# Performance work log

Measured on AMD Instinct MI355X. Metric: run time of the kernel, lower is better.

## Reference

```python
import jax, jax.numpy as jnp
import numpy as np

N = 50000      # nodes
E = 800000     # edges (before self-loops)
IN = 256       # in_channels
HID = 16       # hidden_channels per head
HEADS = 8
OUT = 64       # out_channels (classes)
NEG_SLOPE = 0.2  # PyG GATConv leaky_relu slope


def setup_inputs() -> dict:
    key = jax.random.key(0)
    ks = jax.random.split(key, 10)
    x = jax.random.normal(ks[0], (N, IN), jnp.float32)
    edge_index = jax.random.randint(ks[1], (2, E), 0, N, dtype=jnp.int32)
    g = lambda k, shape: jax.random.normal(k, shape, jnp.float32) * (1.0 / np.sqrt(shape[0]))
    W1 = g(ks[2], (IN, HEADS * HID))
    a_src1 = jax.random.normal(ks[3], (HEADS, HID), jnp.float32) * 0.1
    a_dst1 = jax.random.normal(ks[4], (HEADS, HID), jnp.float32) * 0.1
    b1 = jnp.zeros((HEADS * HID,), jnp.float32)
    W2 = g(ks[5], (HEADS * HID, OUT))
    a_src2 = jax.random.normal(ks[6], (1, OUT), jnp.float32) * 0.1
    a_dst2 = jax.random.normal(ks[7], (1, OUT), jnp.float32) * 0.1
    b2 = jnp.zeros((OUT,), jnp.float32)
    return {"x": x, "edge_index": edge_index, "W1": W1, "a_src1": a_src1,
            "a_dst1": a_dst1, "b1": b1, "W2": W2, "a_src2": a_src2,
            "a_dst2": a_dst2, "b2": b2}


def gat_conv(x, src, dst, W, a_s, a_d, b, heads, concat):
    # x: [n, f]; edges src->dst; attention softmax over incoming edges of dst
    n = x.shape[0]
    h = (x @ W).reshape(n, heads, -1)                 # [n, H, d]
    al_s = jnp.einsum('nhd,hd->nh', h, a_s)           # [n, H]
    al_d = jnp.einsum('nhd,hd->nh', h, a_d)
    e = jax.nn.leaky_relu(al_s[src] + al_d[dst], negative_slope=NEG_SLOPE)  # [E, H]
    m = jax.ops.segment_max(e, dst, num_segments=n)   # stable scatter-softmax
    ex = jnp.exp(e - m[dst])
    den = jax.ops.segment_sum(ex, dst, num_segments=n)
    alpha = ex / (den[dst] + 1e-16)                   # [E, H]
    out = jax.ops.segment_sum(h[src] * alpha[:, :, None], dst, num_segments=n)  # [n, H, d]
    out = out.reshape(n, -1) if concat else out.mean(axis=1)
    return out + b


def reference(x, edge_index, W1, a_src1, a_dst1, b1, W2, a_src2, a_dst2, b2):
    # inference mode: dropout disabled. PyG GATConv adds self-loops by default.
    n = x.shape[0]
    loop = jnp.arange(n, dtype=edge_index.dtype)
    ei = jnp.concatenate([edge_index, jnp.stack([loop, loop])], axis=1)
    src, dst = ei[0], ei[1]
    h = gat_conv(x, src, dst, W1, a_src1, a_dst1, b1, HEADS, True)
    h = jax.nn.elu(h)
    h = gat_conv(h, src, dst, W2, a_src2, a_dst2, b2, 1, False)
    return jax.nn.log_softmax(h, axis=1)
```

## Files before the change

kernel.cpp:

```cpp
#include <hip/hip_runtime.h>
#include <hip/hip_bf16.h>


typedef __attribute__((ext_vector_type(8))) short short8;
typedef __attribute__((ext_vector_type(4))) float f4;
typedef __attribute__((ext_vector_type(2))) float float2v;

#define NCHUNK 64
#define NRANGE 4
#define RSIZE 16384
#define CONVB 80

#define A1PAD 72
#define B1PAD 264
#define G2PAD 136

__device__ __forceinline__ unsigned short f2bf(float f) {
  unsigned int u = __builtin_bit_cast(unsigned int, f);
  u += 0x7fffu + ((u >> 16) & 1u);
  return (unsigned short)(u >> 16);
}
__device__ __forceinline__ float bf2f(unsigned short h) {
  unsigned int u = ((unsigned int)h) << 16;
  return __builtin_bit_cast(float, u);
}

__device__ __forceinline__ unsigned char f2fp8(float f) {
  unsigned int u = __builtin_bit_cast(unsigned int, f);
  unsigned int s = (u >> 24) & 0x80u;
  float a = fabsf(f);
  a = fminf(a, 448.f);
  if (a < 0.015625f) {
    int m = (int)rintf(a * 512.f);
    return (unsigned char)(s | (unsigned)m);
  }
  unsigned int ub = __builtin_bit_cast(unsigned int, a);
  ub += 0xFFFFFu + ((ub >> 20) & 1u);
  unsigned int e = (ub >> 23) - 120u;
  unsigned int m = (ub >> 20) & 7u;
  if (e > 15u) { e = 15u; m = 6u; }
  return (unsigned char)(s | (e << 3) | m);
}

__global__ __launch_bounds__(512) void hist_kernel(const int* __restrict__ ei,
                                                   int* __restrict__ hist,
                                                   const float* __restrict__ W1,
                                                   const float* __restrict__ W2,
                                                   unsigned short* __restrict__ Wt1,
                                                   unsigned short* __restrict__ Wt2,
                                                   int E, int N, int ET, int CS) {
  if (blockIdx.x >= NCHUNK * NRANGE) {
    int i = (blockIdx.x - NCHUNK * NRANGE) * 512 + threadIdx.x;
    if (i < 128 * 256) {
      int n = i >> 8, k = i & 255;
      Wt1[i] = f2bf(W1[k * 128 + n]);
    } else {
      int j = i - 128 * 256;
      if (j < 64 * 128) {
        int n = j >> 7, k = j & 127;
        Wt2[j] = f2bf(W2[k * 64 + n]);
      }
    }
    return;
  }
  __shared__ int lh[RSIZE];
  const int c = blockIdx.x & (NCHUNK - 1);
  const int r = blockIdx.x >> 6;
  const int base = r * RSIZE;
  for (int i = threadIdx.x; i < RSIZE; i += 512) lh[i] = 0;
  __syncthreads();
  const int e0 = c * CS, e1 = min(e0 + CS, ET);
  for (int e = e0 + threadIdx.x; e < e1; e += 512) {
    int d = (e < E) ? ei[E + e] : (e - E);
    unsigned dl = (unsigned)(d - base);
    if (dl < RSIZE) atomicAdd(&lh[dl], 1);
  }
  __syncthreads();
  for (int i = threadIdx.x; i < RSIZE; i += 512) {
    int d = base + i;
    if (d < N) hist[c * N + d] = lh[i];
  }
}

__global__ __launch_bounds__(256) void colscan_kernel(int* __restrict__ hist,
                                                      int* __restrict__ deg, int N) {
  int d = blockIdx.x * 256 + threadIdx.x;
  if (d >= N) return;
  int run = 0;
#pragma unroll 8
  for (int c = 0; c < NCHUNK; ++c) {
    int v = hist[c * N + d];
    hist[c * N + d] = run;
    run += v;
  }
  deg[d] = run;
}

__global__ __launch_bounds__(1024) void scan1_kernel(const int* __restrict__ deg,
                                                     int* __restrict__ rowptr,
                                                     int* __restrict__ bsum, int N) {
  __shared__ int wtot[16];
  const int lane = threadIdx.x & 63, wid = threadIdx.x >> 6;
  int i = blockIdx.x * 1024 + threadIdx.x;
  int v = (i < N) ? deg[i] : 0;
  int incl = v;
#pragma unroll
  for (int off = 1; off < 64; off <<= 1) {
    int t = __shfl_up(incl, off, 64);
    if (lane >= off) incl += t;
  }
  if (lane == 63) wtot[wid] = incl;
  __syncthreads();
  int woff = 0;
#pragma unroll
  for (int w = 0; w < 16; ++w) woff += (w < wid) ? wtot[w] : 0;
  if (i < N) rowptr[i] = woff + incl - v;
  if (threadIdx.x == 1023) bsum[blockIdx.x] = woff + incl;
}

__global__ __launch_bounds__(256) void scan3_kernel(int* __restrict__ rowptr,
                                                    const int* __restrict__ bsum,
                                                    int N, int ET) {
  int lane = threadIdx.x & 63;
  int g = blockIdx.x >> 2;
  int bv = (lane < g) ? bsum[lane] : 0;
#pragma unroll
  for (int off = 32; off; off >>= 1) bv += __shfl_xor(bv, off, 64);
  int i = blockIdx.x * 256 + threadIdx.x;
  if (i < N) rowptr[i] += bv;
  if (i == N) rowptr[N] = ET;
}

__global__ __launch_bounds__(512) void scatter2_kernel(const int* __restrict__ ei,
                                                       const int* __restrict__ hist,
                                                       const int* __restrict__ rowptr,
                                                       int* __restrict__ csr_src,
                                                       int E, int N, int ET, int CS) {
  __shared__ int lh[RSIZE];
  const int c = blockIdx.x & (NCHUNK - 1);
  const int r = blockIdx.x >> 6;
  const int base = r * RSIZE;
  for (int i = threadIdx.x; i < RSIZE; i += 512) {
    int d = base + i;
    lh[i] = (d < N) ? (rowptr[d] + hist[c * N + d]) : 0;
  }
  __syncthreads();
  const int e0 = c * CS, e1 = min(e0 + CS, ET);
  for (int e = e0 + threadIdx.x; e < e1; e += 512) {
    int s, d;
    if (e < E) { s = ei[e]; d = ei[E + e]; }
    else       { s = e - E; d = s; }
    unsigned dl = (unsigned)(d - base);
    if (dl < RSIZE) {
      int slot = atomicAdd(&lh[dl], 1);
      csr_src[slot] = s;
    }
  }
}

__global__ __launch_bounds__(256) void gemm1_mfma(const float* __restrict__ X,
                                                  const unsigned short* __restrict__ Wt,
                                                  const float* __restrict__ as1,
                                                  const float* __restrict__ ad1,
                                                  unsigned char* __restrict__ H,
                                                  float* __restrict__ als,
                                                  float* __restrict__ ald,
                                                  int M) {
  __shared__ unsigned short Bs[64 * B1PAD];
  __shared__ unsigned short As[2][64 * A1PAD];
  const int t = threadIdx.x;
  const int ln = t & 63;
  const int wv = t >> 6;
  const int ml = ln & 15, q = ln >> 4;
  const int ch = blockIdx.x & 1;
  const int rb = (blockIdx.x >> 1) * 64;
  const int r0 = rb + wv * 16;
  const int alr = wv * 16 + ml;

  int srow[4], skg[4];
#pragma unroll
  for (int i = 0; i < 4; ++i) {
    int g = i * 256 + t;
    srow[i] = g >> 4;
    skg[i] = g & 15;
  }

  float4 astg[4];
#pragma unroll
  for (int i = 0; i < 4; ++i)
    astg[i] = *(const float4*)(X + (size_t)min(rb + srow[i], M - 1) * 256 + skg[i] * 4);

#pragma unroll
  for (int i = 0; i < 8; ++i) {
    int g = i * 256 + t;
    int brow = g >> 5, bc = g & 31;
    *(short8*)&Bs[brow * B1PAD + bc * 8] =
        *(const short8*)(Wt + (size_t)(ch * 64 + brow) * 256 + bc * 8);
  }

#pragma unroll
  for (int i = 0; i < 4; ++i) {
    ushort4 pk;
    pk.x = f2bf(astg[i].x); pk.y = f2bf(astg[i].y);
    pk.z = f2bf(astg[i].z); pk.w = f2bf(astg[i].w);
    *(ushort4*)&As[0][srow[i] * A1PAD + skg[i] * 4] = pk;
  }
  __syncthreads();

  f4 acc[4];
#pragma unroll
  for (int b = 0; b < 4; ++b) acc[b] = (f4)0.f;

#pragma unroll
  for (int s = 0; s < 4; ++s) {
    const int buf = s & 1;
    if (s < 3) {
#pragma unroll
      for (int i = 0; i < 4; ++i)
        astg[i] = *(const float4*)(X + (size_t)min(rb + srow[i], M - 1) * 256 +
                                   (s + 1) * 64 + skg[i] * 4);
    }
#pragma unroll
    for (int kk = 0; kk < 2; ++kk) {
      short8 av = *(const short8*)&As[buf][alr * A1PAD + kk * 32 + q * 8];
#pragma unroll
      for (int b = 0; b < 4; ++b) {
        short8 bfr = *(const short8*)&Bs[(b * 16 + ml) * B1PAD + s * 64 + kk * 32 + q * 8];
        acc[b] = __builtin_amdgcn_mfma_f32_16x16x32_bf16(av, bfr, acc[b], 0, 0, 0);
      }
    }
    if (s < 3) {
#pragma unroll
      for (int i = 0; i < 4; ++i) {
        ushort4 pk;
        pk.x = f2bf(astg[i].x); pk.y = f2bf(astg[i].y);
        pk.z = f2bf(astg[i].z); pk.w = f2bf(astg[i].w);
        *(ushort4*)&As[buf ^ 1][srow[i] * A1PAD + skg[i] * 4] = pk;
      }
    }
    __syncthreads();
  }

#pragma unroll
  for (int i = 0; i < 4; ++i) {
    int rr = r0 + q * 4 + i;
    bool ok = rr < M;
    if (ok) {
#pragma unroll
      for (int b = 0; b < 4; ++b)
        H[(size_t)rr * 128 + ch * 64 + b * 16 + ml] = f2fp8(acc[b][i]);
    }
#pragma unroll
    for (int b = 0; b < 4; ++b) {
      float ps = acc[b][i] * as1[ch * 64 + b * 16 + ml];
      float pd = acc[b][i] * ad1[ch * 64 + b * 16 + ml];
#pragma unroll
      for (int off = 1; off < 16; off <<= 1) {
        ps += __shfl_xor(ps, off, 16);
        pd += __shfl_xor(pd, off, 16);
      }
      if (ok && ml == b) {
        als[(size_t)rr * 8 + ch * 4 + b] = ps;
        ald[(size_t)rr * 8 + ch * 4 + b] = pd;
      }
    }
  }
}

__global__ __launch_bounds__(256) void gemm2_mfma(const unsigned short* __restrict__ Xb,
                                                  const unsigned short* __restrict__ Wt,
                                                  const float* __restrict__ as2,
                                                  const float* __restrict__ ad2,
                                                  unsigned char* __restrict__ H,
                                                  float* __restrict__ als,
                                                  float* __restrict__ ald,
                                                  int M) {
  __shared__ unsigned short Asl[64 * G2PAD];
  __shared__ unsigned short Bsl[64 * G2PAD];
  const int t = threadIdx.x;
  const int ln = t & 63;
  const int wv = t >> 6;
  const int ml = ln & 15, q = ln >> 4;
  const int rb = blockIdx.x * 64;
  const int r0 = rb + wv * 16;
  const int alr = wv * 16 + ml;

#pragma unroll
  for (int i = 0; i < 4; ++i) {
    int g = i * 256 + t;
    int row = g >> 4, kg = g & 15;
    *(short8*)&Asl[row * G2PAD + kg * 8] =
        *(const short8*)(Xb + (size_t)min(rb + row, M - 1) * 128 + kg * 8);
    *(short8*)&Bsl[row * G2PAD + kg * 8] =
        *(const short8*)(Wt + (size_t)row * 128 + kg * 8);
  }
  __syncthreads();

  short8 av[4];
#pragma unroll
  for (int s = 0; s < 4; ++s)
    av[s] = *(const short8*)&Asl[alr * G2PAD + s * 32 + q * 8];

  f4 acc[4];
#pragma unroll
  for (int b = 0; b < 4; ++b) acc[b] = (f4)0.f;

#pragma unroll
  for (int s = 0; s < 4; ++s) {
#pragma unroll
    for (int b = 0; b < 4; ++b) {
      short8 bfr = *(const short8*)&Bsl[(b * 16 + ml) * G2PAD + s * 32 + q * 8];
      acc[b] = __builtin_amdgcn_mfma_f32_16x16x32_bf16(av[s], bfr, acc[b], 0, 0, 0);
    }
  }

#pragma unroll
  for (int i = 0; i < 4; ++i) {
    int rr = r0 + q * 4 + i;
    bool ok = rr < M;
    if (ok) {
#pragma unroll
      for (int b = 0; b < 4; ++b)
        H[(size_t)rr * 64 + b * 16 + ml] = f2fp8(acc[b][i]);
    }
    float ps = 0.f, pd = 0.f;
#pragma unroll
    for (int b = 0; b < 4; ++b) {
      ps += acc[b][i] * as2[b * 16 + ml];
      pd += acc[b][i] * ad2[b * 16 + ml];
    }
#pragma unroll
    for (int off = 1; off < 16; off <<= 1) {
      ps += __shfl_xor(ps, off, 16);
      pd += __shfl_xor(pd, off, 16);
    }
    if (ok && ml == 0) { als[rr] = ps; ald[rr] = pd; }
  }
}

__global__ __launch_bounds__(256) void attn1_kernel(
    const unsigned char* __restrict__ h1, const float* __restrict__ als,
    const float* __restrict__ ald, const float* __restrict__ b1,
    const int* __restrict__ rowptr, const int* __restrict__ csr_src,
    unsigned short* __restrict__ helu, int N) {
  int d = __builtin_amdgcn_readfirstlane(
      (blockIdx.x * blockDim.x + threadIdx.x) >> 6);
  int lane = threadIdx.x & 63;
  if (d >= N) return;
  const int hh = lane >> 3;
  const int hw = lane & 7;
  const int ew = lane >> 3;
  const float aldp = ald[d * 8 + hw];
  const int beg = rowptr[d], end = rowptr[d + 1];
  const unsigned char* h1l = h1 + 2 * lane;
  float den = 0.f, ax = 0.f, ay = 0.f;

  int idx0 = beg + ew;
  int se = csr_src[idx0 < end ? idx0 : end - 1];
  for (int p0 = beg; p0 < end; p0 += 8) {
    int p1 = p0 + 8;
    int se_n = se;
    if (p1 < end) {
      int idx1 = p1 + ew;
      se_n = csr_src[idx1 < end ? idx1 : end - 1];
    }
    float v = als[se * 8 + hw] + aldp;
    v = fmaxf(v, 0.2f * v);
    float w = ((p0 + ew) < end) ? __expf(v) : 0.f;
    int sjv[8];
#pragma unroll
    for (int j = 0; j < 8; ++j) sjv[j] = __shfl(se, j * 8);
    unsigned short pkv[8];
#pragma unroll
    for (int j = 0; j < 8; ++j)
      pkv[j] = *(const unsigned short*)(h1l + (size_t)sjv[j] * 128);
#pragma unroll
    for (int j = 0; j < 8; ++j) {
      float wj = __shfl(w, j * 8 + hh);
      float2v g = __builtin_amdgcn_cvt_pk_f32_fp8(pkv[j], false);
      den += wj; ax += wj * g.x; ay += wj * g.y;
    }
    se = se_n;
  }

  float inv = 1.0f / (den + 1e-16f);
  float2 bb = *(const float2*)(b1 + 2 * lane);
  float o0 = ax * inv + bb.x;
  float o1 = ay * inv + bb.y;
  o0 = o0 > 0.f ? o0 : __expf(o0) - 1.0f;
  o1 = o1 > 0.f ? o1 : __expf(o1) - 1.0f;
  ushort2 ov; ov.x = f2bf(o0); ov.y = f2bf(o1);
  *(ushort2*)(helu + (size_t)d * 128 + 2 * lane) = ov;
}

__global__ __launch_bounds__(256) void attn2_kernel(
    const unsigned char* __restrict__ h2, const float* __restrict__ als,
    const float* __restrict__ ald, const float* __restrict__ b2,
    const int* __restrict__ rowptr, const int* __restrict__ csr_src,
    float* __restrict__ out, int N) {
  int d = __builtin_amdgcn_readfirstlane(
      (blockIdx.x * blockDim.x + threadIdx.x) >> 6);
  int lane = threadIdx.x & 63;
  if (d >= N) return;
  const float aldd = ald[d];
  const int beg = rowptr[d], end = rowptr[d + 1];
  const unsigned char* h2l = h2 + lane;
  float den = 0.f, acc = 0.f;

  int idx0 = beg + lane;
  int se = csr_src[idx0 < end ? idx0 : end - 1];
  for (int p0 = beg; p0 < end; p0 += 64) {
    int p1 = p0 + 64;
    int se_n = se;
    if (p1 < end) {
      int i1 = p1 + lane;
      se_n = csr_src[i1 < end ? i1 : end - 1];
    }
    float v = als[se] + aldd;
    v = fmaxf(v, 0.2f * v);
    float w = ((p0 + lane) < end) ? __expf(v) : 0.f;
    int cnt = min(64, end - p0);
    for (int j0 = 0; j0 < cnt; j0 += 8) {
      int sjv[8];
#pragma unroll
      for (int j = 0; j < 8; ++j) sjv[j] = __shfl(se, j0 + j);
      float gv[8];
#pragma unroll
      for (int j = 0; j < 8; ++j)
        gv[j] = __builtin_amdgcn_cvt_f32_fp8(h2l[(size_t)sjv[j] * 64], 0);
#pragma unroll
      for (int j = 0; j < 8; ++j) {
        float wj = __shfl(w, j0 + j);
        den += wj; acc += wj * gv[j];
      }
    }
    se = se_n;
  }

  float z = acc / (den + 1e-16f) + b2[lane];
  float zm = z;
#pragma unroll
  for (int off = 32; off; off >>= 1) zm = fmaxf(zm, __shfl_xor(zm, off, 64));
  float ex = __expf(z - zm), se2 = ex;
#pragma unroll
  for (int off = 32; off; off >>= 1) se2 += __shfl_xor(se2, off, 64);
  out[(size_t)d * 64 + lane] = z - zm - __logf(se2);
}

extern "C" void kernel_launch(void* const* d_in, const int* in_sizes, int n_in,
                              void* d_out, int out_size, void* d_ws, size_t ws_size,
                              hipStream_t stream) {
  const int N = in_sizes[0] / 256;
  const int E = in_sizes[1] / 2;
  const int ET = E + N;
  const int CS = (ET + NCHUNK - 1) / NCHUNK;
  const int NB = (N + 1023) / 1024;

  const float* x   = (const float*)d_in[0];
  const int*   ei  = (const int*)d_in[1];
  const float* W1  = (const float*)d_in[2];
  const float* as1 = (const float*)d_in[3];
  const float* ad1 = (const float*)d_in[4];
  const float* b1  = (const float*)d_in[5];
  const float* W2  = (const float*)d_in[6];
  const float* as2 = (const float*)d_in[7];
  const float* ad2 = (const float*)d_in[8];
  const float* b2  = (const float*)d_in[9];
  float* out = (float*)d_out;

  char* p = (char*)d_ws;
  unsigned char* h1f8 = (unsigned char*)p; p += (size_t)N * 128;
  unsigned char* h2f8 = h1f8;
  unsigned short* helu = (unsigned short*)p; p += (size_t)NCHUNK * N * 4;
  int* hist = (int*)helu;
  unsigned short* Wt1  = (unsigned short*)p; p += (size_t)128 * 256 * 2;
  unsigned short* Wt2  = (unsigned short*)p; p += (size_t)64 * 128 * 2;
  float* als1 = (float*)p; p += (size_t)N * 8 * 4;
  float* ald1 = (float*)p; p += (size_t)N * 8 * 4;
  float* als2 = (float*)p; p += (size_t)N * 4;
  float* ald2 = (float*)p; p += (size_t)N * 4;
  int* deg     = (int*)p; p += (size_t)N * 4;
  int* rowptr  = (int*)p; p += (size_t)(N + 1) * 4;
  int* bsum    = (int*)p; p += 64 * 4;
  int* csr_src = (int*)p; p += (size_t)ET * 4;

  hist_kernel<<<NCHUNK * NRANGE + CONVB, 512, 0, stream>>>(ei, hist, W1, W2, Wt1, Wt2,
                                                           E, N, ET, CS);
  colscan_kernel<<<(N + 255) / 256, 256, 0, stream>>>(hist, deg, N);
  scan1_kernel<<<NB, 1024, 0, stream>>>(deg, rowptr, bsum, N);
  scan3_kernel<<<(N + 256) / 256, 256, 0, stream>>>(rowptr, bsum, N, ET);
  scatter2_kernel<<<NCHUNK * NRANGE, 512, 0, stream>>>(ei, hist, rowptr, csr_src, E, N, ET, CS);

  gemm1_mfma<<<2 * ((N + 63) / 64), 256, 0, stream>>>(x, Wt1, as1, ad1, h1f8, als1, ald1, N);
  attn1_kernel<<<(N + 3) / 4, 256, 0, stream>>>(h1f8, als1, ald1, b1, rowptr, csr_src, helu, N);

  gemm2_mfma<<<(N + 63) / 64, 256, 0, stream>>>(helu, Wt2, as2, ad2, h2f8, als2, ald2, N);
  attn2_kernel<<<(N + 3) / 4, 256, 0, stream>>>(h2f8, als2, ald2, b2, rowptr, csr_src, out, N);
}
```

Before: 247.6 us.

## Fuse column scan into block scan and shrink histogram to 16-bit

Removes the separate colscan kernel by doing the per-node chunk prefix inside scan1, dropping one launch and the deg buffer. The per-chunk histogram is stored as unsigned short instead of int, halving its memory traffic in hist, scan and scatter kernels. Per-chunk counts fit easily in 16 bits, but a single destination node collecting more than 65535 edges in one chunk would overflow. scan1 now runs with 49 blocks of 1024 threads, each doing a 64-step strided loop, which may reduce parallelism compared with the old 196-block colscan.

```diff
diff --git a/kernel.cpp b/kernel.cpp
--- a/kernel.cpp
+++ b/kernel.cpp
@@ -43,7 +43,7 @@
 }
 
 __global__ __launch_bounds__(512) void hist_kernel(const int* __restrict__ ei,
-                                                   int* __restrict__ hist,
+                                                   unsigned short* __restrict__ hist,
                                                    const float* __restrict__ W1,
                                                    const float* __restrict__ W2,
                                                    unsigned short* __restrict__ Wt1,
@@ -78,31 +78,27 @@
   __syncthreads();
   for (int i = threadIdx.x; i < RSIZE; i += 512) {
     int d = base + i;
-    if (d < N) hist[c * N + d] = lh[i];
-  }
-}
-
-__global__ __launch_bounds__(256) void colscan_kernel(int* __restrict__ hist,
-                                                      int* __restrict__ deg, int N) {
-  int d = blockIdx.x * 256 + threadIdx.x;
-  if (d >= N) return;
-  int run = 0;
-#pragma unroll 8
-  for (int c = 0; c < NCHUNK; ++c) {
-    int v = hist[c * N + d];
-    hist[c * N + d] = run;
-    run += v;
-  }
-  deg[d] = run;
-}
-
-__global__ __launch_bounds__(1024) void scan1_kernel(const int* __restrict__ deg,
+    if (d < N) hist[c * N + d] = (unsigned short)lh[i];
+  }
+}
+
+__global__ __launch_bounds__(1024) void scan1_kernel(unsigned short* __restrict__ hist,
                                                      int* __restrict__ rowptr,
                                                      int* __restrict__ bsum, int N) {
   __shared__ int wtot[16];
   const int lane = threadIdx.x & 63, wid = threadIdx.x >> 6;
   int i = blockIdx.x * 1024 + threadIdx.x;
-  int v = (i < N) ? deg[i] : 0;
+  int v = 0;
+  if (i < N) {
+    int run = 0;
+#pragma unroll 8
+    for (int c = 0; c < NCHUNK; ++c) {
+      int cv = hist[c * N + i];
+      hist[c * N + i] = (unsigned short)run;
+      run += cv;
+    }
+    v = run;
+  }
   int incl = v;
 #pragma unroll
   for (int off = 1; off < 64; off <<= 1) {
@@ -132,7 +128,7 @@
 }
 
 __global__ __launch_bounds__(512) void scatter2_kernel(const int* __restrict__ ei,
-                                                       const int* __restrict__ hist,
+                                                       const unsigned short* __restrict__ hist,
                                                        const int* __restrict__ rowptr,
                                                        int* __restrict__ csr_src,
                                                        int E, int N, int ET, int CS) {
@@ -471,23 +467,21 @@
   char* p = (char*)d_ws;
   unsigned char* h1f8 = (unsigned char*)p; p += (size_t)N * 128;
   unsigned char* h2f8 = h1f8;
-  unsigned short* helu = (unsigned short*)p; p += (size_t)NCHUNK * N * 4;
-  int* hist = (int*)helu;
+  unsigned short* helu = (unsigned short*)p; p += (size_t)N * 128 * 2;
+  unsigned short* hist = helu;
   unsigned short* Wt1  = (unsigned short*)p; p += (size_t)128 * 256 * 2;
   unsigned short* Wt2  = (unsigned short*)p; p += (size_t)64 * 128 * 2;
   float* als1 = (float*)p; p += (size_t)N * 8 * 4;
   float* ald1 = (float*)p; p += (size_t)N * 8 * 4;
   float* als2 = (float*)p; p += (size_t)N * 4;
   float* ald2 = (float*)p; p += (size_t)N * 4;
-  int* deg     = (int*)p; p += (size_t)N * 4;
   int* rowptr  = (int*)p; p += (size_t)(N + 1) * 4;
   int* bsum    = (int*)p; p += 64 * 4;
   int* csr_src = (int*)p; p += (size_t)ET * 4;
 
   hist_kernel<<<NCHUNK * NRANGE + CONVB, 512, 0, stream>>>(ei, hist, W1, W2, Wt1, Wt2,
                                                            E, N, ET, CS);
-  colscan_kernel<<<(N + 255) / 256, 256, 0, stream>>>(hist, deg, N);
-  scan1_kernel<<<NB, 1024, 0, stream>>>(deg, rowptr, bsum, N);
+  scan1_kernel<<<NB, 1024, 0, stream>>>(hist, rowptr, bsum, N);
   scan3_kernel<<<(N + 256) / 256, 256, 0, stream>>>(rowptr, bsum, N, ET);
   scatter2_kernel<<<NCHUNK * NRANGE, 512, 0, stream>>>(ei, hist, rowptr, csr_src, E, N, ET, CS);
 
```

Result: no change. 246.3 us (-0.5%).
